# Kernel optimization log

Hardware: AMD Instinct MI355X
Metric: run time of the kernel (lower is better)

Reference implementation:

```python
import jax, jax.numpy as jnp
import numpy as np

D_MODEL = 512
NUM_HEADS = 8
HEAD_DIM = D_MODEL // NUM_HEADS
EPS = 1e-6


def setup_inputs() -> dict:
    key = jax.random.key(0)
    ks = jax.random.split(key, 9)
    s = 1.0 / np.sqrt(D_MODEL)
    x = jax.random.normal(ks[0], (4, 8192, D_MODEL), dtype=jnp.float32)
    Wq = jax.random.uniform(ks[1], (D_MODEL, D_MODEL), jnp.float32, -s, s)
    bq = jax.random.uniform(ks[2], (D_MODEL,), jnp.float32, -s, s)
    Wk = jax.random.uniform(ks[3], (D_MODEL, D_MODEL), jnp.float32, -s, s)
    bk = jax.random.uniform(ks[4], (D_MODEL,), jnp.float32, -s, s)
    Wv = jax.random.uniform(ks[5], (D_MODEL, D_MODEL), jnp.float32, -s, s)
    bv = jax.random.uniform(ks[6], (D_MODEL,), jnp.float32, -s, s)
    Wo = jax.random.uniform(ks[7], (D_MODEL, D_MODEL), jnp.float32, -s, s)
    bo = jax.random.uniform(ks[8], (D_MODEL,), jnp.float32, -s, s)
    return {"x": x, "Wq": Wq, "bq": bq, "Wk": Wk, "bk": bk,
            "Wv": Wv, "bv": bv, "Wo": Wo, "bo": bo}


def _feature_map(t):
    # ELU(x) + 1
    return jax.nn.elu(t) + 1.0


def reference(x, Wq, bq, Wk, bk, Wv, bv, Wo, bo):
    B, N, C = x.shape
    H, D = NUM_HEADS, HEAD_DIM
    # projections: torch Linear computes x @ W.T + b
    q = (x @ Wq.T + bq).reshape(B, N, H, D).transpose(0, 2, 1, 3)  # [B,H,N,D]
    k = (x @ Wk.T + bk).reshape(B, N, H, D).transpose(0, 2, 1, 3)
    v = (x @ Wv.T + bv).reshape(B, N, H, D).transpose(0, 2, 1, 3)
    q = _feature_map(q)
    k = _feature_map(k)
    # kv: [B,H,D,D] = k^T v   (global, non-causal linear attention)
    kv = jnp.einsum('bhnd,bhne->bhde', k, v)
    # normalizer: q . sum_n(k)  -> [B,H,N,1]
    k_sum = k.sum(axis=2)  # [B,H,D]
    z = jnp.einsum('bhnd,bhd->bhn', q, k_sum)[..., None] + EPS
    out = jnp.einsum('bhnd,bhde->bhne', q, kv) / z  # [B,H,N,D]
    out = out.transpose(0, 2, 1, 3).reshape(B, N, C)
    return out @ Wo.T + bo
```

## Files before the change

kernel.cpp:

```cpp
#include <hip/hip_runtime.h>
#include <hip/hip_bf16.h>

typedef __attribute__((ext_vector_type(8))) short short8;
typedef __attribute__((ext_vector_type(4))) float f32x4;
typedef unsigned short u16;
typedef unsigned int u32;

#define T_TOK 32768
#define CDIM  512
#define HEADS 8
#define HD    64
#define NSEQ  8192

__device__ __forceinline__ u16 f2bf(float f) {
  u32 u = __builtin_bit_cast(u32, f);
  u = u + 0x7fffu + ((u >> 16) & 1u);
  return (u16)(u >> 16);
}
__device__ __forceinline__ float bf2f(u16 s) {
  return __builtin_bit_cast(float, ((u32)s) << 16);
}

__global__ __launch_bounds__(256) void k_convx(const float* __restrict__ x,
                                               u16* __restrict__ xb) {
  size_t i = (size_t)blockIdx.x * 256 + threadIdx.x;
  size_t stride = (size_t)gridDim.x * 256;
  size_t total = (size_t)T_TOK * 512 / 8;
  for (; i < total; i += stride) {
    float4 a = *reinterpret_cast<const float4*>(&x[i * 8]);
    float4 b = *reinterpret_cast<const float4*>(&x[i * 8 + 4]);
    ushort4 r0, r1;
    r0.x = f2bf(a.x); r0.y = f2bf(a.y); r0.z = f2bf(a.z); r0.w = f2bf(a.w);
    r1.x = f2bf(b.x); r1.y = f2bf(b.y); r1.z = f2bf(b.z); r1.w = f2bf(b.w);
    *reinterpret_cast<ushort4*>(&xb[i * 8])     = r0;
    *reinterpret_cast<ushort4*>(&xb[i * 8 + 4]) = r1;
  }
}

__global__ void k_pack_w(const float* __restrict__ Wq, const float* __restrict__ Wk,
                         const float* __restrict__ Wv, const float* __restrict__ Wo,
                         u16* __restrict__ Wcat) {
  int idx = blockIdx.x * 256 + threadIdx.x;
  int c = idx & 511;
  int o2 = idx >> 9;
  const float* W = (o2 < 512) ? Wq : (o2 < 1024) ? Wk : (o2 < 1536) ? Wv : Wo;
  int o = o2 & 511;
  Wcat[idx] = f2bf(W[o * 512 + c]);
}

template<int MODE>
__global__ __launch_bounds__(512, 2) void k_gemm(const u16* __restrict__ Ag,
    const u16* __restrict__ Wcat,
    const float* __restrict__ b0, const float* __restrict__ b1, const float* __restrict__ b2,
    u16* __restrict__ obf, float* __restrict__ of32) {
  constexpr int NT = (MODE == 0) ? 6 : 2;
  constexpr int BROW = (MODE == 0) ? 0 : 1536;
  constexpr int OSTRIDE = (MODE == 0) ? 1536 : 512;
  __shared__ u16 As[2][256][64];
  __shared__ u16 Bs[2][256][64];
  int bid = blockIdx.x;
  constexpr int GRID = (T_TOK / 256) * NT;
  constexpr int CHUNK = GRID / 8;
  int swz = (bid & 7) * CHUNK + (bid >> 3);
  int m0 = (swz / NT) * 256;
  int n0 = (swz % NT) * 256;
  int tid = threadIdx.x;
  int lane = tid & 63, w = tid >> 6;
  int wr = w >> 2, wc = w & 3;
  f32x4 acc_a[4][4], acc_b[4][4];
  _Pragma("unroll")
  for (int i = 0; i < 4; ++i)
    _Pragma("unroll")
    for (int j = 0; j < 4; ++j) { acc_a[i][j] = (f32x4)0.0f; acc_b[i][j] = (f32x4)0.0f; }

  const u16* Bg = Wcat + (size_t)BROW * 512;
  int grl = lane >> 3;
  int gcl = (((lane & 7) ^ grl)) * 8;
  int l15 = lane & 15, lhi = lane >> 4, sx = lane & 7;

#define STAGE(buf, k0)                                                                     \
  _Pragma("unroll")                                                                        \
  for (int i = 0; i < 4; ++i) {                                                            \
    int r = i * 64 + w * 8;                                                                \
    __builtin_amdgcn_global_load_lds(                                                      \
        (const __attribute__((address_space(1))) void*)&Ag[(size_t)(m0 + r + grl) * 512 + (k0) + gcl], \
        (__attribute__((address_space(3))) void*)&As[buf][r][0], 16, 0, 0);                \
    __builtin_amdgcn_global_load_lds(                                                      \
        (const __attribute__((address_space(1))) void*)&Bg[(size_t)(n0 + r + grl) * 512 + (k0) + gcl], \
        (__attribute__((address_space(3))) void*)&Bs[buf][r][0], 16, 0, 0);                \
  }

#define COMPUTE(buf)                                                                       \
  _Pragma("unroll")                                                                        \
  for (int kk = 0; kk < 2; ++kk) {                                                         \
    int slot = (kk * 4 + lhi) ^ sx;                                                        \
    short8 bfr[4];                                                                         \
    _Pragma("unroll")                                                                      \
    for (int n = 0; n < 4; ++n)                                                            \
      bfr[n] = *reinterpret_cast<const short8*>(&Bs[buf][wc * 64 + n * 16 + l15][slot * 8]);\
    {                                                                                      \
      short8 af[4];                                                                        \
      _Pragma("unroll")                                                                    \
      for (int m = 0; m < 4; ++m)                                                          \
        af[m] = *reinterpret_cast<const short8*>(&As[buf][wr * 128 + m * 16 + l15][slot * 8]); \
      __builtin_amdgcn_s_setprio(1);                                                       \
      _Pragma("unroll")                                                                    \
      for (int m = 0; m < 4; ++m)                                                          \
        _Pragma("unroll")                                                                  \
        for (int n = 0; n < 4; ++n)                                                        \
          acc_a[m][n] = __builtin_amdgcn_mfma_f32_16x16x32_bf16(af[m], bfr[n], acc_a[m][n], 0, 0, 0); \
      __builtin_amdgcn_s_setprio(0);                                                       \
    }                                                                                      \
    {                                                                                      \
      short8 af[4];                                                                        \
      _Pragma("unroll")                                                                    \
      for (int m = 0; m < 4; ++m)                                                          \
        af[m] = *reinterpret_cast<const short8*>(&As[buf][wr * 128 + 64 + m * 16 + l15][slot * 8]); \
      __builtin_amdgcn_s_setprio(1);                                                       \
      _Pragma("unroll")                                                                    \
      for (int m = 0; m < 4; ++m)                                                          \
        _Pragma("unroll")                                                                  \
        for (int n = 0; n < 4; ++n)                                                        \
          acc_b[m][n] = __builtin_amdgcn_mfma_f32_16x16x32_bf16(af[m], bfr[n], acc_b[m][n], 0, 0, 0); \
      __builtin_amdgcn_s_setprio(0);                                                       \
    }                                                                                      \
  }

  STAGE(0, 0)
  STAGE(1, 64)
  asm volatile("s_waitcnt vmcnt(8)" ::: "memory");
  __builtin_amdgcn_s_barrier();
  _Pragma("unroll")
  for (int t = 0; t < 7; ++t) {
    COMPUTE(t & 1)
    __builtin_amdgcn_s_barrier();
    if (t < 6) {
      STAGE(t & 1, (t + 2) * 64)
      asm volatile("s_waitcnt vmcnt(8)" ::: "memory");
    } else {
      asm volatile("s_waitcnt vmcnt(0)" ::: "memory");
    }
    __builtin_amdgcn_s_barrier();
  }
  COMPUTE(1)
#undef STAGE
#undef COMPUTE

  _Pragma("unroll")
  for (int m = 0; m < 4; ++m) {
    _Pragma("unroll")
    for (int half = 0; half < 2; ++half) {
      int row = m0 + wr * 128 + half * 64 + m * 16 + lhi * 4;
      _Pragma("unroll")
      for (int n = 0; n < 4; ++n) {
        int col = n0 + wc * 64 + n * 16 + l15;
        float bias;
        if (MODE == 0)
          bias = (col < 512) ? b0[col] : (col < 1024) ? b1[col - 512] : b2[col - 1024];
        else
          bias = b0[col];
        _Pragma("unroll")
        for (int j = 0; j < 4; ++j) {
          float vv = (half == 0 ? acc_a[m][n][j] : acc_b[m][n][j]) + bias;
          if (MODE == 0) {
            if (col < 1024) vv = (vv > 0.0f) ? (vv + 1.0f) : __expf(vv);
            obf[(size_t)(row + j) * OSTRIDE + col] = f2bf(vv);
          } else {
            of32[(size_t)(row + j) * OSTRIDE + col] = vv;
          }
        }
      }
    }
  }
}

__global__ __launch_bounds__(256) void k_kvstats(const u16* __restrict__ qkv,
    float* __restrict__ kvp, float* __restrict__ ksp) {
  __shared__ u16 kt[64][32];
  __shared__ u16 vt[64][32];
  __shared__ float ks_red[4][64];
  int hh = blockIdx.x;
  int s  = blockIdx.y;
  int b = hh >> 3, h = hh & 7;
  int tid = threadIdx.x;
  int lane = tid & 63, w = tid >> 6;
  size_t tbase = (size_t)b * NSEQ + (size_t)s * 512;
  f32x4 acc[4];
  for (int n = 0; n < 4; ++n) acc[n] = (f32x4)0.0f;
  float ksum_loc = 0.0f;
  int kcol = 512 + h * 64;
  int vcol = 1024 + h * 64;
  int l15 = lane & 15;
  int rsw = 8 * (l15 >> 2);

  for (int step = 0; step < 16; ++step) {
    size_t t0 = tbase + (size_t)step * 32;
    for (int jj = 0; jj < 4; ++jj) {
      int id = tid + 256 * jj;
      int trow = (id >> 4) & 31;
      int dq = id & 15;
      int isv = id >> 9;
      ushort4 val = *reinterpret_cast<const ushort4*>(
          &qkv[(t0 + trow) * 1536 + (isv ? vcol : kcol) + dq * 4]);
      u16 (*dst)[32] = isv ? vt : kt;
      int colw = trow ^ (8 * (dq & 3));
      dst[dq * 4 + 0][colw] = val.x;
      dst[dq * 4 + 1][colw] = val.y;
      dst[dq * 4 + 2][colw] = val.z;
      dst[dq * 4 + 3][colw] = val.w;
    }
    __syncthreads();
    {
      int d = tid & 63, g = tid >> 6;
      int gs = 8 * (g ^ ((d >> 2) & 3));
      float sl = 0;
      for (int i = 0; i < 8; ++i) sl += bf2f(kt[d][gs + i]);
      ksum_loc += sl;
    }
    int kb = 8 * (lane >> 4);
    short8 af = *reinterpret_cast<const short8*>(&kt[w * 16 + l15][kb ^ rsw]);
    for (int n = 0; n < 4; ++n) {
      short8 bfr = *reinterpret_cast<const short8*>(&vt[n * 16 + l15][kb ^ rsw]);
      acc[n] = __builtin_amdgcn_mfma_f32_16x16x32_bf16(af, bfr, acc[n], 0, 0, 0);
    }
    __syncthreads();
  }
  size_t pbase = ((size_t)hh * 16 + s) * 4096;
  for (int n = 0; n < 4; ++n) {
    int d = w * 16 + (lane >> 4) * 4;
    int e = n * 16 + (lane & 15);
    for (int j = 0; j < 4; ++j)
      kvp[pbase + (size_t)(d + j) * 64 + e] = acc[n][j];
  }
  ks_red[tid >> 6][tid & 63] = ksum_loc;
  __syncthreads();
  if (tid < 64) {
    float r = ks_red[0][tid] + ks_red[1][tid] + ks_red[2][tid] + ks_red[3][tid];
    ksp[((size_t)hh * 16 + s) * 64 + tid] = r;
  }
}

__global__ void k_reduce(const float* __restrict__ kvp, const float* __restrict__ ksp,
                         u16* __restrict__ kvb, float* __restrict__ ksum) {
  int hh = blockIdx.x;
  int sl = blockIdx.y;
  int tid = threadIdx.x;
  for (int j = 0; j < 2; ++j) {
    int idx = sl * 512 + tid + 256 * j;
    float a = 0;
    for (int s = 0; s < 16; ++s) a += kvp[((size_t)hh * 16 + s) * 4096 + idx];
    int d = idx >> 6, e = idx & 63;
    kvb[(size_t)hh * 4096 + e * 64 + d] = f2bf(a);
  }
  if (sl == 0 && tid < 64) {
    float a = 0;
    for (int s = 0; s < 16; ++s) a += ksp[((size_t)hh * 16 + s) * 64 + tid];
    ksum[hh * 64 + tid] = a;
  }
}

__global__ __launch_bounds__(256) void k_attn(const u16* __restrict__ qkv,
    const u16* __restrict__ kvb, const float* __restrict__ ksum,
    u16* __restrict__ attn) {
  __shared__ u16 qf[32][520];
  __shared__ float zl[32][8];
  __shared__ float kss[8][64];
  int tid = threadIdx.x;
  int lane = tid & 63, w = tid >> 6;
  size_t t0 = (size_t)blockIdx.x * 32;
  int b = (int)(t0 >> 13);
  for (int jj = 0; jj < 16; ++jj) {
    int id = tid + 256 * jj;
    int row = id >> 7, cq = id & 127;
    *reinterpret_cast<ushort4*>(&qf[row][cq * 4]) =
        *reinterpret_cast<const ushort4*>(&qkv[(t0 + row) * 1536 + cq * 4]);
  }
  { int i = tid, i2 = tid + 256;
    kss[i >> 6][i & 63]   = ksum[b * 512 + i];
    kss[i2 >> 6][i2 & 63] = ksum[b * 512 + i2]; }
  __syncthreads();
  {
    int tok = tid & 31, h = tid >> 5;
    float z = 0;
    for (int jq = 0; jq < 8; ++jq) {
      short8 qv = *reinterpret_cast<const short8*>(&qf[tok][h * 64 + jq * 8]);
      for (int e = 0; e < 8; ++e) z += bf2f((u16)qv[e]) * kss[h][jq * 8 + e];
    }
    zl[tok][h] = z + 1e-6f;
  }
  __syncthreads();
  for (int hi = 0; hi < 2; ++hi) {
    int h = w * 2 + hi;
    size_t kvoff = (size_t)(b * 8 + h) * 4096;
    f32x4 acc[2][4];
    for (int m = 0; m < 2; ++m) for (int n = 0; n < 4; ++n) acc[m][n] = (f32x4)0.0f;
    for (int kk = 0; kk < 2; ++kk) {
      int kb = kk * 32 + 8 * (lane >> 4);
      short8 af[2], bfr[4];
      for (int m = 0; m < 2; ++m)
        af[m] = *reinterpret_cast<const short8*>(&qf[m * 16 + (lane & 15)][h * 64 + kb]);
      for (int n = 0; n < 4; ++n)
        bfr[n] = *reinterpret_cast<const short8*>(&kvb[kvoff + (size_t)(n * 16 + (lane & 15)) * 64 + kb]);
      for (int m = 0; m < 2; ++m)
        for (int n = 0; n < 4; ++n)
          acc[m][n] = __builtin_amdgcn_mfma_f32_16x16x32_bf16(af[m], bfr[n], acc[m][n], 0, 0, 0);
    }
    for (int m = 0; m < 2; ++m) {
      int tokb = m * 16 + (lane >> 4) * 4;
      for (int n = 0; n < 4; ++n) {
        int e = n * 16 + (lane & 15);
        for (int j = 0; j < 4; ++j) {
          float vv = acc[m][n][j] / zl[tokb + j][h];
          attn[(t0 + tokb + j) * 512 + h * 64 + e] = f2bf(vv);
        }
      }
    }
  }
}

extern "C" void kernel_launch(void* const* d_in, const int* in_sizes, int n_in,
                              void* d_out, int out_size, void* d_ws, size_t ws_size,
                              hipStream_t stream) {
  const float* x  = (const float*)d_in[0];
  const float* Wq = (const float*)d_in[1];
  const float* bq = (const float*)d_in[2];
  const float* Wk = (const float*)d_in[3];
  const float* bk = (const float*)d_in[4];
  const float* Wv = (const float*)d_in[5];
  const float* bv = (const float*)d_in[6];
  const float* Wo = (const float*)d_in[7];
  const float* bo = (const float*)d_in[8];
  float* out = (float*)d_out;

  char* ws = (char*)d_ws;
  u16*   Wcat = (u16*)(ws + 0);
  u16*   qkv  = (u16*)(ws + 2097152);
  u16*   xb   = (u16*)(ws + 102760448);
  float* kvp  = (float*)(ws + 102760448);
  u16*   attn = (u16*)(ws + 102760448);
  float* ksp  = (float*)(ws + 136314880);
  u16*   kvb  = (u16*)(ws + 136445952);
  float* ksum = (float*)(ws + 136708096);

  k_convx  <<<2048, 256, 0, stream>>>(x, xb);
  k_pack_w <<<4096, 256, 0, stream>>>(Wq, Wk, Wv, Wo, Wcat);
  k_gemm<0><<<768, 512, 0, stream>>>(xb, Wcat, bq, bk, bv, qkv, nullptr);
  k_kvstats<<<dim3(32, 16), 256, 0, stream>>>(qkv, kvp, ksp);
  k_reduce <<<dim3(32, 8), 256, 0, stream>>>(kvp, ksp, kvb, ksum);
  k_attn   <<<1024, 256, 0, stream>>>(qkv, kvb, ksum, attn);
  k_gemm<1><<<256, 512, 0, stream>>>(attn, Wcat, bo, nullptr, nullptr, nullptr, out);
}
```

Measured before the change: 171.8 us.

## Split GEMM K-tiles into halves with fine-grained interleaved load/MFMA phases

Restructures the projection GEMM main loop. Each 64-wide K tile is split into two 32-wide halves in LDS, and the schedule is unrolled into phases where each phase issues one async global-to-LDS load group while running a 4x4 MFMA block, separated by barriers. This spreads memory traffic across compute and drops the XOR swizzle in favour of a plain 32-wide layout. The risks are more barriers per tile and possible LDS bank conflicts from the unswizzled layout.

Result: slower. 180.3 us, median of 2 (+4.9%).

```diff
diff --git a/kernel.cpp b/kernel.cpp
--- a/kernel.cpp
+++ b/kernel.cpp
@@ -11,6 +11,9 @@
 #define HEADS 8
 #define HD    64
 #define NSEQ  8192
+
+#define AS1 __attribute__((address_space(1)))
+#define AS3 __attribute__((address_space(3)))
 
 __device__ __forceinline__ u16 f2bf(float f) {
   u32 u = __builtin_bit_cast(u32, f);
@@ -56,8 +59,8 @@
   constexpr int NT = (MODE == 0) ? 6 : 2;
   constexpr int BROW = (MODE == 0) ? 0 : 1536;
   constexpr int OSTRIDE = (MODE == 0) ? 1536 : 512;
-  __shared__ u16 As[2][256][64];
-  __shared__ u16 Bs[2][256][64];
+  __shared__ u16 As[2][2][256][32];
+  __shared__ u16 Bs[2][2][256][32];
   int bid = blockIdx.x;
   constexpr int GRID = (T_TOK / 256) * NT;
   constexpr int CHUNK = GRID / 8;
@@ -74,77 +77,72 @@
     for (int j = 0; j < 4; ++j) { acc_a[i][j] = (f32x4)0.0f; acc_b[i][j] = (f32x4)0.0f; }
 
   const u16* Bg = Wcat + (size_t)BROW * 512;
-  int grl = lane >> 3;
-  int gcl = (((lane & 7) ^ grl)) * 8;
-  int l15 = lane & 15, lhi = lane >> 4, sx = lane & 7;
-
-#define STAGE(buf, k0)                                                                     \
-  _Pragma("unroll")                                                                        \
-  for (int i = 0; i < 4; ++i) {                                                            \
-    int r = i * 64 + w * 8;                                                                \
+  int l15 = lane & 15, lhi = lane >> 4;
+  int grow = w * 16 + (lane >> 2);
+  int gk   = (lane & 3) * 8;
+
+#define SA(d, h, t)                                                                        \
+  _Pragma("unroll") for (int j_ = 0; j_ < 2; ++j_)                                         \
     __builtin_amdgcn_global_load_lds(                                                      \
-        (const __attribute__((address_space(1))) void*)&Ag[(size_t)(m0 + r + grl) * 512 + (k0) + gcl], \
-        (__attribute__((address_space(3))) void*)&As[buf][r][0], 16, 0, 0);                \
+        (const AS1 void*)&Ag[(size_t)(m0 + j_ * 128 + grow) * 512 + (t) * 64 + (h) * 32 + gk], \
+        (AS3 void*)&As[d][h][j_ * 128 + w * 16][0], 16, 0, 0);
+#define SB(d, h, t)                                                                        \
+  _Pragma("unroll") for (int j_ = 0; j_ < 2; ++j_)                                         \
     __builtin_amdgcn_global_load_lds(                                                      \
-        (const __attribute__((address_space(1))) void*)&Bg[(size_t)(n0 + r + grl) * 512 + (k0) + gcl], \
-        (__attribute__((address_space(3))) void*)&Bs[buf][r][0], 16, 0, 0);                \
-  }
-
-#define COMPUTE(buf)                                                                       \
-  _Pragma("unroll")                                                                        \
-  for (int kk = 0; kk < 2; ++kk) {                                                         \
-    int slot = (kk * 4 + lhi) ^ sx;                                                        \
-    short8 bfr[4];                                                                         \
-    _Pragma("unroll")                                                                      \
-    for (int n = 0; n < 4; ++n)                                                            \
-      bfr[n] = *reinterpret_cast<const short8*>(&Bs[buf][wc * 64 + n * 16 + l15][slot * 8]);\
-    {                                                                                      \
-      short8 af[4];                                                                        \
-      _Pragma("unroll")                                                                    \
-      for (int m = 0; m < 4; ++m)                                                          \
-        af[m] = *reinterpret_cast<const short8*>(&As[buf][wr * 128 + m * 16 + l15][slot * 8]); \
-      __builtin_amdgcn_s_setprio(1);                                                       \
-      _Pragma("unroll")                                                                    \
-      for (int m = 0; m < 4; ++m)                                                          \
-        _Pragma("unroll")                                                                  \
-        for (int n = 0; n < 4; ++n)                                                        \
-          acc_a[m][n] = __builtin_amdgcn_mfma_f32_16x16x32_bf16(af[m], bfr[n], acc_a[m][n], 0, 0, 0); \
-      __builtin_amdgcn_s_setprio(0);                                                       \
-    }                                                                                      \
-    {                                                                                      \
-      short8 af[4];                                                                        \
-      _Pragma("unroll")                                                                    \
-      for (int m = 0; m < 4; ++m)                                                          \
-        af[m] = *reinterpret_cast<const short8*>(&As[buf][wr * 128 + 64 + m * 16 + l15][slot * 8]); \
-      __builtin_amdgcn_s_setprio(1);                                                       \
-      _Pragma("unroll")                                                                    \
-      for (int m = 0; m < 4; ++m)                                                          \
-        _Pragma("unroll")                                                                  \
-        for (int n = 0; n < 4; ++n)                                                        \
-          acc_b[m][n] = __builtin_amdgcn_mfma_f32_16x16x32_bf16(af[m], bfr[n], acc_b[m][n], 0, 0, 0); \
-      __builtin_amdgcn_s_setprio(0);                                                       \
-    }                                                                                      \
-  }
-
-  STAGE(0, 0)
-  STAGE(1, 64)
-  asm volatile("s_waitcnt vmcnt(8)" ::: "memory");
+        (const AS1 void*)&Bg[(size_t)(n0 + j_ * 128 + grow) * 512 + (t) * 64 + (h) * 32 + gk], \
+        (AS3 void*)&Bs[d][h][j_ * 128 + w * 16][0], 16, 0, 0);
+#define VW(n) asm volatile("s_waitcnt vmcnt(" #n ")" ::: "memory");
+
+#define PH0(d, kk, ...) {                                                                  \
+    _Pragma("unroll") for (int m = 0; m < 4; ++m)                                          \
+      af[m] = *reinterpret_cast<const short8*>(&As[d][kk][wr * 128 + m * 16 + l15][lhi * 8]); \
+    _Pragma("unroll") for (int n = 0; n < 4; ++n)                                          \
+      bfr[n] = *reinterpret_cast<const short8*>(&Bs[d][kk][wc * 64 + n * 16 + l15][lhi * 8]); \
+    __VA_ARGS__                                                                            \
+    __builtin_amdgcn_s_barrier();                                                          \
+    __builtin_amdgcn_s_setprio(1);                                                         \
+    _Pragma("unroll") for (int m = 0; m < 4; ++m)                                          \
+      _Pragma("unroll") for (int n = 0; n < 4; ++n)                                        \
+        acc_a[m][n] = __builtin_amdgcn_mfma_f32_16x16x32_bf16(af[m], bfr[n], acc_a[m][n], 0, 0, 0); \
+    __builtin_amdgcn_s_setprio(0);                                                         \
+    __builtin_amdgcn_s_barrier(); }
+#define PH1(d, kk, ...) {                                                                  \
+    _Pragma("unroll") for (int m = 0; m < 4; ++m)                                          \
+      af[m] = *reinterpret_cast<const short8*>(&As[d][kk][wr * 128 + 64 + m * 16 + l15][lhi * 8]); \
+    __VA_ARGS__                                                                            \
+    __builtin_amdgcn_s_barrier();                                                          \
+    __builtin_amdgcn_s_setprio(1);                                                         \
+    _Pragma("unroll") for (int m = 0; m < 4; ++m)                                          \
+      _Pragma("unroll") for (int n = 0; n < 4; ++n)                                        \
+        acc_b[m][n] = __builtin_amdgcn_mfma_f32_16x16x32_bf16(af[m], bfr[n], acc_b[m][n], 0, 0, 0); \
+    __builtin_amdgcn_s_setprio(0);                                                         \
+    __builtin_amdgcn_s_barrier(); }
+
+  short8 af[4], bfr[4];
+  SA(0, 0, 0) SB(0, 0, 0) SA(0, 1, 0) SB(0, 1, 0) SA(1, 0, 1) SB(1, 0, 1)
+  VW(4)
   __builtin_amdgcn_s_barrier();
-  _Pragma("unroll")
-  for (int t = 0; t < 7; ++t) {
-    COMPUTE(t & 1)
-    __builtin_amdgcn_s_barrier();
-    if (t < 6) {
-      STAGE(t & 1, (t + 2) * 64)
-      asm volatile("s_waitcnt vmcnt(8)" ::: "memory");
-    } else {
-      asm volatile("s_waitcnt vmcnt(0)" ::: "memory");
-    }
-    __builtin_amdgcn_s_barrier();
-  }
-  COMPUTE(1)
-#undef STAGE
-#undef COMPUTE
+  PH0(0, 0, SA(1, 1, 1)) PH1(0, 0, SB(1, 1, 1))
+  PH0(0, 1, SA(0, 0, 2)) PH1(0, 1, SB(0, 0, 2) VW(4))
+  PH0(1, 0, SA(0, 1, 2)) PH1(1, 0, SB(0, 1, 2))
+  PH0(1, 1, SA(1, 0, 3)) PH1(1, 1, SB(1, 0, 3) VW(4))
+  PH0(0, 0, SA(1, 1, 3)) PH1(0, 0, SB(1, 1, 3))
+  PH0(0, 1, SA(0, 0, 4)) PH1(0, 1, SB(0, 0, 4) VW(4))
+  PH0(1, 0, SA(0, 1, 4)) PH1(1, 0, SB(0, 1, 4))
+  PH0(1, 1, SA(1, 0, 5)) PH1(1, 1, SB(1, 0, 5) VW(4))
+  PH0(0, 0, SA(1, 1, 5)) PH1(0, 0, SB(1, 1, 5))
+  PH0(0, 1, SA(0, 0, 6)) PH1(0, 1, SB(0, 0, 6) VW(4))
+  PH0(1, 0, SA(0, 1, 6)) PH1(1, 0, SB(0, 1, 6))
+  PH0(1, 1, SA(1, 0, 7)) PH1(1, 1, SB(1, 0, 7) VW(4))
+  PH0(0, 0, SA(1, 1, 7)) PH1(0, 0, SB(1, 1, 7))
+  PH0(0, 1, )            PH1(0, 1, VW(0))
+  PH0(1, 0, )            PH1(1, 0, )
+  PH0(1, 1, )            PH1(1, 1, )
+#undef SA
+#undef SB
+#undef VW
+#undef PH0
+#undef PH1
 
   _Pragma("unroll")
   for (int m = 0; m < 4; ++m) {
```
